# Optimization experiments

Measured on AMD Instinct MI355X. Metric: run time of the kernel, lower is better.

The kernel has to match this reference:

```python
import jax, jax.numpy as jnp
import numpy as np

N, D = 8192, 256
TEMP = 0.07


def setup_inputs() -> dict:
    key = jax.random.key(0)
    kx, ky = jax.random.split(key)
    x = jax.random.normal(kx, (N, D), dtype=jnp.float32)
    y = jax.random.normal(ky, (N, D), dtype=jnp.float32)
    # L2-normalize (standard for InfoNCE; keeps exp(sim/temp) finite)
    x = x / jnp.linalg.norm(x, axis=-1, keepdims=True)
    y = y / jnp.linalg.norm(y, axis=-1, keepdims=True)
    return {"x": x, "y": y}


def reference(x, y):
    # sim_matrix = exp(x @ y^T / temperature), shape [N, N]
    sim = jnp.exp(jnp.matmul(x, y.T) / TEMP)
    # positives: exp(<x_i, y_i>/T) == diagonal of sim
    l_pos = jnp.exp(jnp.sum(x * y, axis=-1) / TEMP)
    # negatives: row-sum excluding the diagonal (equivalent to masked_select)
    l_neg = jnp.sum(sim, axis=-1) - jnp.diagonal(sim)
    loss = jnp.mean(-jnp.log(l_pos / l_neg))
    return loss
```

## Files before the change

### kernel.cpp

```cpp
#include <hip/hip_runtime.h>
#include <hip/hip_bf16.h>

#define N_ROWS 8192
#define D_DIM  256

static constexpr float kQuantScale = 64.0f;
static constexpr float kScaleAcc = 20.609929155556627f / 4096.0f;
static constexpr float kInvTAcc  = 14.285714285714286f / 4096.0f;

typedef float f32x4 __attribute__((ext_vector_type(4)));
typedef int   i32x4 __attribute__((ext_vector_type(4)));
typedef int   i32x8 __attribute__((ext_vector_type(8)));

__device__ __forceinline__ void gl_lds16(const void* g, void* l) {
  __builtin_amdgcn_global_load_lds(
      (const __attribute__((address_space(1))) void*)g,
      (__attribute__((address_space(3))) void*)l, 16, 0, 0);
}

__global__ __launch_bounds__(256)
void cvt_fp8_kernel(const float* __restrict__ x, const float* __restrict__ y,
                    unsigned char* __restrict__ xq, unsigned char* __restrict__ yq,
                    float* __restrict__ rowsum, unsigned int* __restrict__ done,
                    float* __restrict__ out) {
  if (blockIdx.x == 0) {
    for (int i = threadIdx.x; i < N_ROWS; i += 256) rowsum[i] = 0.f;
    if (threadIdx.x < 32) done[threadIdx.x] = 0u;
    if (threadIdx.x == 32) out[0] = 0.f;
  }
  const int per_mat = N_ROWS * D_DIM / 8;
  int idx = blockIdx.x * blockDim.x + threadIdx.x;
  const float* src = x;
  unsigned char* dst = xq;
  int i = idx;
  if (idx >= per_mat) { src = y; dst = yq; i = idx - per_mat; }
  float4 a = ((const float4*)src)[2 * (size_t)i];
  float4 b = ((const float4*)src)[2 * (size_t)i + 1];
  int v0 = 0, v1 = 0;
  v0 = __builtin_amdgcn_cvt_pk_fp8_f32(a.x * kQuantScale, a.y * kQuantScale, v0, false);
  v0 = __builtin_amdgcn_cvt_pk_fp8_f32(a.z * kQuantScale, a.w * kQuantScale, v0, true);
  v1 = __builtin_amdgcn_cvt_pk_fp8_f32(b.x * kQuantScale, b.y * kQuantScale, v1, false);
  v1 = __builtin_amdgcn_cvt_pk_fp8_f32(b.z * kQuantScale, b.w * kQuantScale, v1, true);
  *(int2*)(dst + (size_t)i * 8) = make_int2(v0, v1);
}

__global__ __launch_bounds__(512, 1)
void infonce_gemm(const unsigned char* __restrict__ X,
                  const unsigned char* __restrict__ Y,
                  float* __restrict__ rowsum, float* __restrict__ diag,
                  unsigned int* __restrict__ done, float* __restrict__ out) {
  __shared__ unsigned char Xs[256 * 256];
  __shared__ unsigned char Ys[2][128 * 256];
  __shared__ unsigned int ticket_s;

  const int b  = blockIdx.x;
  const int bi = b >> 3;
  const int gj = b & 7;

  const int t    = threadIdx.x;
  const int lane = t & 63;
  const int wave = t >> 6;
  const int wm   = wave >> 1;
  const int wn   = wave & 1;
  const int quad = lane >> 4;
  const int l15  = lane & 15;

  const unsigned char* Xblk = X + (size_t)(bi * 256) * D_DIM;

#pragma unroll
  for (int it = 0; it < 8; ++it) {
    const int c0  = (it * 8 + wave) * 64;
    const int s   = c0 + lane;
    const int row = s >> 4;
    const int cg  = (s & 15) ^ (row & 15);
    gl_lds16(Xblk + (size_t)row * D_DIM + cg * 16, &Xs[c0 * 16]);
  }
  {
    const unsigned char* Yblk = Y + (size_t)(gj * 8) * 128 * D_DIM;
#pragma unroll
    for (int it = 0; it < 4; ++it) {
      const int c0  = (it * 8 + wave) * 64;
      const int s   = c0 + lane;
      const int row = s >> 4;
      const int cg  = (s & 15) ^ (row & 15);
      gl_lds16(Yblk + (size_t)row * D_DIM + cg * 16, &Ys[0][c0 * 16]);
    }
  }

  __syncthreads();

  i32x8 a8r[2][4];
#pragma unroll
  for (int kb = 0; kb < 2; ++kb) {
#pragma unroll
    for (int mt = 0; mt < 4; ++mt) {
      const int row = wm * 64 + mt * 16 + l15;
      const int p0  = (kb * 8 + quad * 2 + 0) ^ (row & 15);
      const int p1  = (kb * 8 + quad * 2 + 1) ^ (row & 15);
      i32x4 lo = *(const i32x4*)(&Xs[row * 256 + p0 * 16]);
      i32x4 hi = *(const i32x4*)(&Xs[row * 256 + p1 * 16]);
      a8r[kb][mt] = __builtin_shufflevector(lo, hi, 0, 1, 2, 3, 4, 5, 6, 7);
    }
  }

  f32x4 acc[4][4];
#pragma unroll
  for (int a = 0; a < 4; ++a)
#pragma unroll
    for (int c = 0; c < 4; ++c) acc[a][c] = (f32x4){0.f, 0.f, 0.f, 0.f};

  float psum[4][4];
#pragma unroll
  for (int a = 0; a < 4; ++a)
#pragma unroll
    for (int c = 0; c < 4; ++c) psum[a][c] = 0.f;

  for (int tt = 0; tt < 8; ++tt) {
    const int p = tt & 1;

    if (tt) __syncthreads();

    if (tt < 7) {
      const unsigned char* Yblk = Y + (size_t)(gj * 8 + tt + 1) * 128 * D_DIM;
#pragma unroll
      for (int it = 0; it < 4; ++it) {
        const int c0  = (it * 8 + wave) * 64;
        const int s   = c0 + lane;
        const int row = s >> 4;
        const int cg  = (s & 15) ^ (row & 15);
        gl_lds16(Yblk + (size_t)row * D_DIM + cg * 16, &Ys[p ^ 1][c0 * 16]);
      }
    }

#pragma unroll
    for (int kb = 0; kb < 2; ++kb) {
      i32x8 b8[4];
#pragma unroll
      for (int nt = 0; nt < 4; ++nt) {
        const int row = wn * 64 + nt * 16 + l15;
        const int p0  = (kb * 8 + quad * 2 + 0) ^ (row & 15);
        const int p1  = (kb * 8 + quad * 2 + 1) ^ (row & 15);
        i32x4 lo = *(const i32x4*)(&Ys[p][row * 256 + p0 * 16]);
        i32x4 hi = *(const i32x4*)(&Ys[p][row * 256 + p1 * 16]);
        b8[nt] = __builtin_shufflevector(lo, hi, 0, 1, 2, 3, 4, 5, 6, 7);
      }
#pragma unroll
      for (int mt = 0; mt < 4; ++mt)
#pragma unroll
        for (int nt = 0; nt < 4; ++nt)
          acc[mt][nt] = __builtin_amdgcn_mfma_scale_f32_16x16x128_f8f6f4(
              a8r[kb][mt], b8[nt], acc[mt][nt],
              0, 0,
              0, 0x7F7F7F7F,
              0, 0x7F7F7F7F);
    }

#pragma unroll
    for (int mt = 0; mt < 4; ++mt) {
#pragma unroll
      for (int rr = 0; rr < 4; ++rr) {
        float part = 0.f;
#pragma unroll
        for (int nt = 0; nt < 4; ++nt)
          part += __builtin_amdgcn_exp2f(acc[mt][nt][rr] * kScaleAcc);
        psum[mt][rr] += part;
      }
    }
    {
      const int ct = gj * 8 + tt;
      const bool d0 = (ct == 2 * bi)     && (wm == wn);
      const bool d1 = (ct == 2 * bi + 1) && (wm == wn + 2);
      if (d0 || d1) {
        const int gi_base = bi * 256 + wm * 64;
#pragma unroll
        for (int nt = 0; nt < 4; ++nt)
#pragma unroll
          for (int rr = 0; rr < 4; ++rr)
            if (l15 == quad * 4 + rr)
              atomicExch(&diag[gi_base + nt * 16 + l15], acc[nt][nt][rr]);
      }
    }
#pragma unroll
    for (int a = 0; a < 4; ++a)
#pragma unroll
      for (int c = 0; c < 4; ++c) acc[a][c] = (f32x4){0.f, 0.f, 0.f, 0.f};
  }

  {
    const int gi_base = bi * 256 + wm * 64;
#pragma unroll
    for (int mt = 0; mt < 4; ++mt) {
#pragma unroll
      for (int rr = 0; rr < 4; ++rr) {
        float v = psum[mt][rr];
        v += __shfl_xor(v, 1);
        v += __shfl_xor(v, 2);
        v += __shfl_xor(v, 4);
        v += __shfl_xor(v, 8);
        if (l15 == 0)
          atomicAdd(&rowsum[gi_base + mt * 16 + quad * 4 + rr], v);
      }
    }
  }

  __syncthreads();
  if (t == 0) ticket_s = atomicAdd(&done[bi], 1u);
  __syncthreads();
  if (ticket_s == 7u) {
    __threadfence();
    float local = 0.f;
    if (t < 256) {
      const int i = bi * 256 + t;
      const float rs = atomicAdd(&rowsum[i], 0.0f);
      const float d  = atomicAdd(&diag[i], 0.0f);
      local = __logf(rs - __builtin_amdgcn_exp2f(d * kScaleAcc)) - d * kInvTAcc;
    }
    local += __shfl_down(local, 32);
    local += __shfl_down(local, 16);
    local += __shfl_down(local, 8);
    local += __shfl_down(local, 4);
    local += __shfl_down(local, 2);
    local += __shfl_down(local, 1);
    float* red = (float*)Xs;
    if (lane == 0) red[wave] = local;
    __syncthreads();
    if (t == 0) {
      float s = 0.f;
#pragma unroll
      for (int w = 0; w < 8; ++w) s += red[w];
      atomicAdd(out, s / (float)N_ROWS);
    }
  }
}

extern "C" void kernel_launch(void* const* d_in, const int* in_sizes, int n_in,
                              void* d_out, int out_size, void* d_ws, size_t ws_size,
                              hipStream_t stream) {
  const float* x = (const float*)d_in[0];
  const float* y = (const float*)d_in[1];
  float* out = (float*)d_out;

  float* rowsum = (float*)d_ws;
  float* diag   = rowsum + N_ROWS;
  unsigned int* done = (unsigned int*)(diag + N_ROWS);
  unsigned char* xq = (unsigned char*)d_ws + 2 * N_ROWS * sizeof(float) + 128;
  unsigned char* yq = xq + (size_t)N_ROWS * D_DIM;

  int cvt_blocks = 2 * N_ROWS * D_DIM / 8 / 256;
  cvt_fp8_kernel<<<cvt_blocks, 256, 0, stream>>>(x, y, xq, yq, rowsum, done, out);

  infonce_gemm<<<256, 512, 0, stream>>>(xq, yq, rowsum, diag, done, out);
}
```

Measured before the change: 105.0 us.

## Load X fragments directly into registers and widen fp8 conversion per thread

The GEMM kernel no longer stages the 256x256 X tile through LDS. Each wave loads its A fragments straight from global memory into registers, which removes 64KB of LDS per block and the barrier plus LDS reads that came before the first MFMA. The conversion kernel now handles 16 floats per thread with a 16-byte store instead of 8 floats with an 8-byte store, halving the block count. In exchange, the direct global loads are uncoalesced 16-byte reads, and the per-iteration barrier is now unconditional.

```diff
diff --git a/kernel.cpp b/kernel.cpp
--- a/kernel.cpp
+++ b/kernel.cpp
@@ -28,20 +28,26 @@
     if (threadIdx.x < 32) done[threadIdx.x] = 0u;
     if (threadIdx.x == 32) out[0] = 0.f;
   }
-  const int per_mat = N_ROWS * D_DIM / 8;
+  const int per_mat = N_ROWS * D_DIM / 16;
   int idx = blockIdx.x * blockDim.x + threadIdx.x;
   const float* src = x;
   unsigned char* dst = xq;
   int i = idx;
   if (idx >= per_mat) { src = y; dst = yq; i = idx - per_mat; }
-  float4 a = ((const float4*)src)[2 * (size_t)i];
-  float4 b = ((const float4*)src)[2 * (size_t)i + 1];
-  int v0 = 0, v1 = 0;
+  float4 a = ((const float4*)src)[4 * (size_t)i + 0];
+  float4 b = ((const float4*)src)[4 * (size_t)i + 1];
+  float4 c = ((const float4*)src)[4 * (size_t)i + 2];
+  float4 d = ((const float4*)src)[4 * (size_t)i + 3];
+  int v0 = 0, v1 = 0, v2 = 0, v3 = 0;
   v0 = __builtin_amdgcn_cvt_pk_fp8_f32(a.x * kQuantScale, a.y * kQuantScale, v0, false);
   v0 = __builtin_amdgcn_cvt_pk_fp8_f32(a.z * kQuantScale, a.w * kQuantScale, v0, true);
   v1 = __builtin_amdgcn_cvt_pk_fp8_f32(b.x * kQuantScale, b.y * kQuantScale, v1, false);
   v1 = __builtin_amdgcn_cvt_pk_fp8_f32(b.z * kQuantScale, b.w * kQuantScale, v1, true);
-  *(int2*)(dst + (size_t)i * 8) = make_int2(v0, v1);
+  v2 = __builtin_amdgcn_cvt_pk_fp8_f32(c.x * kQuantScale, c.y * kQuantScale, v2, false);
+  v2 = __builtin_amdgcn_cvt_pk_fp8_f32(c.z * kQuantScale, c.w * kQuantScale, v2, true);
+  v3 = __builtin_amdgcn_cvt_pk_fp8_f32(d.x * kQuantScale, d.y * kQuantScale, v3, false);
+  v3 = __builtin_amdgcn_cvt_pk_fp8_f32(d.z * kQuantScale, d.w * kQuantScale, v3, true);
+  ((int4*)dst)[i] = make_int4(v0, v1, v2, v3);
 }
 
 __global__ __launch_bounds__(512, 1)
@@ -49,7 +55,6 @@
                   const unsigned char* __restrict__ Y,
                   float* __restrict__ rowsum, float* __restrict__ diag,
                   unsigned int* __restrict__ done, float* __restrict__ out) {
-  __shared__ unsigned char Xs[256 * 256];
   __shared__ unsigned char Ys[2][128 * 256];
   __shared__ unsigned int ticket_s;
 
@@ -67,14 +72,19 @@
 
   const unsigned char* Xblk = X + (size_t)(bi * 256) * D_DIM;
 
-#pragma unroll
-  for (int it = 0; it < 8; ++it) {
-    const int c0  = (it * 8 + wave) * 64;
-    const int s   = c0 + lane;
-    const int row = s >> 4;
-    const int cg  = (s & 15) ^ (row & 15);
-    gl_lds16(Xblk + (size_t)row * D_DIM + cg * 16, &Xs[c0 * 16]);
-  }
+  i32x8 a8r[2][4];
+#pragma unroll
+  for (int kb = 0; kb < 2; ++kb) {
+#pragma unroll
+    for (int mt = 0; mt < 4; ++mt) {
+      const size_t off = (size_t)(wm * 64 + mt * 16 + l15) * D_DIM + kb * 128 + quad * 32;
+      i32x4 lo = *(const i32x4*)(Xblk + off);
+      i32x4 hi = *(const i32x4*)(Xblk + off + 16);
+      a8r[kb][mt] = __builtin_shufflevector(lo, hi, 0, 1, 2, 3, 4, 5, 6, 7);
+      asm volatile("" : "+v"(a8r[kb][mt]));
+    }
+  }
+
   {
     const unsigned char* Yblk = Y + (size_t)(gj * 8) * 128 * D_DIM;
 #pragma unroll
@@ -87,22 +97,6 @@
     }
   }
 
-  __syncthreads();
-
-  i32x8 a8r[2][4];
-#pragma unroll
-  for (int kb = 0; kb < 2; ++kb) {
-#pragma unroll
-    for (int mt = 0; mt < 4; ++mt) {
-      const int row = wm * 64 + mt * 16 + l15;
-      const int p0  = (kb * 8 + quad * 2 + 0) ^ (row & 15);
-      const int p1  = (kb * 8 + quad * 2 + 1) ^ (row & 15);
-      i32x4 lo = *(const i32x4*)(&Xs[row * 256 + p0 * 16]);
-      i32x4 hi = *(const i32x4*)(&Xs[row * 256 + p1 * 16]);
-      a8r[kb][mt] = __builtin_shufflevector(lo, hi, 0, 1, 2, 3, 4, 5, 6, 7);
-    }
-  }
-
   f32x4 acc[4][4];
 #pragma unroll
   for (int a = 0; a < 4; ++a)
@@ -118,7 +112,7 @@
   for (int tt = 0; tt < 8; ++tt) {
     const int p = tt & 1;
 
-    if (tt) __syncthreads();
+    __syncthreads();
 
     if (tt < 7) {
       const unsigned char* Yblk = Y + (size_t)(gj * 8 + tt + 1) * 128 * D_DIM;
@@ -221,7 +215,7 @@
     local += __shfl_down(local, 4);
     local += __shfl_down(local, 2);
     local += __shfl_down(local, 1);
-    float* red = (float*)Xs;
+    float* red = (float*)Ys;
     if (lane == 0) red[wave] = local;
     __syncthreads();
     if (t == 0) {
@@ -246,7 +240,7 @@
   unsigned char* xq = (unsigned char*)d_ws + 2 * N_ROWS * sizeof(float) + 128;
   unsigned char* yq = xq + (size_t)N_ROWS * D_DIM;
 
-  int cvt_blocks = 2 * N_ROWS * D_DIM / 8 / 256;
+  int cvt_blocks = 2 * N_ROWS * D_DIM / 16 / 256;
   cvt_fp8_kernel<<<cvt_blocks, 256, 0, stream>>>(x, y, xq, yq, rowsum, done, out);
 
   infonce_gemm<<<256, 512, 0, stream>>>(xq, yq, rowsum, diag, done, out);
```

Result: slower. 107.8 us (+2.6%).
